# Performance work log

Hardware: AMD Instinct MI355X
Metric: run time of the kernel (lower is better)

The kernel has to match this reference:

```python
import jax, jax.numpy as jnp
import numpy as np

B, S, H, D = 16, 64, 16, 16          # batch, seq, heads, head_dim
E = H * D                             # 256
HID = 128                             # attn_hidden_dim


def setup_inputs() -> dict:
    key = jax.random.key(0)
    ks = jax.random.split(key, 12)
    g = lambda k, sh, s: (jax.random.normal(k, sh, dtype=jnp.float32) * s)
    sE = 1.0 / np.sqrt(E)
    s2d = 1.0 / np.sqrt(2 * D)
    sSD = 1.0 / np.sqrt(S * D)
    return {
        "x": jax.random.normal(ks[0], (B, S, E), dtype=jnp.float32),
        "Wq": g(ks[1], (E, E), sE), "bq": g(ks[2], (E,), sE),
        "Wk": g(ks[3], (E, E), sE), "bk": g(ks[4], (E,), sE),
        "Wv": g(ks[5], (E, E), sE), "bv": g(ks[6], (E,), sE),
        "Wa": g(ks[7], (HID, 2 * D), s2d), "ba": g(ks[8], (HID,), s2d),
        "attn_v": jax.random.normal(ks[9], (HID,), dtype=jnp.float32),
        "Wfc": g(ks[10], (E, S * D), sSD), "bfc": g(ks[11], (E,), sSD),
    }


def reference(x, Wq, bq, Wk, bk, Wv, bv, Wa, ba, attn_v, Wfc, bfc):
    b, s, e = x.shape
    q = (x @ Wq.T + bq).reshape(b, s, H, D)
    k = (x @ Wk.T + bk).reshape(b, s, H, D)
    v = (x @ Wv.T + bv).reshape(b, s, H, D)
    # attn_fc(concat(q_i, k_j)) == q_i @ Wa[:, :D].T + k_j @ Wa[:, D:].T + ba
    pre_q = jnp.einsum('bihd,cd->bihc', q, Wa[:, :D]) + ba   # [B,S,H,HID]
    pre_k = jnp.einsum('bjhd,cd->bjhc', k, Wa[:, D:])        # [B,S,H,HID]
    # scores[b,i,j,h] = tanh(pre_q + pre_k) . attn_v
    t = jnp.tanh(pre_q[:, :, None, :, :] + pre_k[:, None, :, :, :])  # [B,S,S,H,HID]
    scores = jnp.einsum('bijhc,c->bijh', t, attn_v)                   # [B,S,S,H]
    w = jax.nn.softmax(scores, axis=2)                                # softmax over key dim
    # faithful to torch.matmul(w[B,S,S,H], v[B,S,H,D]) -> contracts heads
    ctx = jnp.einsum('bqkh,bqhd->bqkd', w, v).reshape(b, s, s * D)    # [B,S,S*D]
    return ctx @ Wfc.T + bfc                                          # [B,S,E]
```

## Files before the change

### kernel.cpp

```cpp
#include <hip/hip_runtime.h>

#define BB 16
#define SS 64
#define HH 16
#define DD 16
#define EE 256
#define HIDD 128

typedef float f32x4 __attribute__((ext_vector_type(4)));

#define K2CONST 2.8853900817779268f
#define L2E 1.4426950408889634f

#define WQ_OFF 0
#define WK_OFF 4160
#define WV_OFF 8320
#define WA_OFF 12480
#define EQT_OFF 17088
#define EKL_OFF 25408
#define QL_OFF 33856
#define KL_OFF 35136
#define AV2_OFF 36416
#define KBA_OFF 36544
#define SM_TOT 36672
#define SL_OFF 0

__global__ __launch_bounds__(512) void k1(
    const float* __restrict__ x,
    const float* __restrict__ Wq, const float* __restrict__ bq,
    const float* __restrict__ Wk, const float* __restrict__ bk,
    const float* __restrict__ Wv, const float* __restrict__ bv,
    const float* __restrict__ Wa, const float* __restrict__ ba,
    const float* __restrict__ attnv,
    float* __restrict__ v_ws, float* __restrict__ w_ws)
{
  __shared__ float sm[SM_TOT];
  const int t = threadIdx.x;
  const int bid = blockIdx.x;
  const int b = bid >> 4;
  const int h = bid & (HH - 1);

  for (int idx = t; idx < 16 * EE; idx += 512) {
    const int r = idx >> 8;
    const int e = idx & 255;
    const size_t g = (size_t)(h * DD + r) * EE + e;
    sm[WQ_OFF + r * 260 + e] = Wq[g];
    sm[WK_OFF + r * 260 + e] = Wk[g];
    sm[WV_OFF + r * 260 + e] = Wv[g];
  }
  for (int idx = t; idx < HIDD * 2 * DD; idx += 512)
    sm[WA_OFF + (idx >> 5) * 36 + (idx & 31)] = Wa[idx];
  if (t < HIDD) {
    sm[AV2_OFF + t] = 2.0f * attnv[t];
    sm[KBA_OFF + t] = K2CONST * ba[t];
  }
  __syncthreads();

  {
    const int i = t >> 3;
    const int dl = t & 7;
    float aq0 = 0.f, aq1 = 0.f, ak0 = 0.f, ak1 = 0.f, av0 = 0.f, av1 = 0.f;
    const float* xr = x + (size_t)(b * SS + i) * EE;
    const float* wq0 = &sm[WQ_OFF + dl * 260];
    const float* wq1 = &sm[WQ_OFF + (dl + 8) * 260];
    const float* wk0 = &sm[WK_OFF + dl * 260];
    const float* wk1 = &sm[WK_OFF + (dl + 8) * 260];
    const float* wv0 = &sm[WV_OFF + dl * 260];
    const float* wv1 = &sm[WV_OFF + (dl + 8) * 260];
#pragma unroll 4
    for (int e = 0; e < EE; e += 4) {
      const f32x4 x4 = *(const f32x4*)(xr + e);
      const f32x4 q04 = *(const f32x4*)(wq0 + e);
      const f32x4 q14 = *(const f32x4*)(wq1 + e);
      const f32x4 k04 = *(const f32x4*)(wk0 + e);
      const f32x4 k14 = *(const f32x4*)(wk1 + e);
      const f32x4 v04 = *(const f32x4*)(wv0 + e);
      const f32x4 v14 = *(const f32x4*)(wv1 + e);
#pragma unroll
      for (int u = 0; u < 4; ++u) {
        aq0 = fmaf(x4[u], q04[u], aq0);
        aq1 = fmaf(x4[u], q14[u], aq1);
        ak0 = fmaf(x4[u], k04[u], ak0);
        ak1 = fmaf(x4[u], k14[u], ak1);
        av0 = fmaf(x4[u], v04[u], av0);
        av1 = fmaf(x4[u], v14[u], av1);
      }
    }
    sm[QL_OFF + i * 20 + dl]     = aq0 + bq[h * DD + dl];
    sm[QL_OFF + i * 20 + dl + 8] = aq1 + bq[h * DD + dl + 8];
    sm[KL_OFF + i * 20 + dl]     = ak0 + bk[h * DD + dl];
    sm[KL_OFF + i * 20 + dl + 8] = ak1 + bk[h * DD + dl + 8];
    v_ws[(size_t)(b * SS + i) * EE + h * DD + dl]     = av0 + bv[h * DD + dl];
    v_ws[(size_t)(b * SS + i) * EE + h * DD + dl + 8] = av1 + bv[h * DD + dl + 8];
  }
  __syncthreads();

  {
    const int i = t >> 3;
    const int cg = t & 7;
    f32x4 q4[4], k4[4];
#pragma unroll
    for (int u = 0; u < 4; ++u) {
      q4[u] = *(const f32x4*)&sm[QL_OFF + i * 20 + u * 4];
      k4[u] = *(const f32x4*)&sm[KL_OFF + i * 20 + u * 4];
    }
#pragma unroll 2
    for (int jj = 0; jj < 16; ++jj) {
      const int c = cg + 8 * jj;
      const float* war = &sm[WA_OFF + c * 36];
      float sq = 0.f, sk = 0.f;
#pragma unroll
      for (int u = 0; u < 4; ++u) {
        const f32x4 a4 = *(const f32x4*)(war + u * 4);
        const f32x4 b4 = *(const f32x4*)(war + 16 + u * 4);
#pragma unroll
        for (int w = 0; w < 4; ++w) {
          sq = fmaf(q4[u][w], a4[w], sq);
          sk = fmaf(k4[u][w], b4[w], sk);
        }
      }
      const float eq = __builtin_amdgcn_exp2f(fmaf(K2CONST, sq, sm[KBA_OFF + c]));
      const float ek = __builtin_amdgcn_exp2f(K2CONST * sk);
      sm[EQT_OFF + c * 65 + i] = eq;
      sm[EKL_OFF + i * 132 + c] = ek;
    }
  }
  __syncthreads();

  {
    const int i = t & 63;
    const int j0 = (t >> 6) << 3;
    float acc[8];
#pragma unroll
    for (int jj = 0; jj < 8; ++jj) acc[jj] = 0.f;
#pragma unroll 2
    for (int c = 0; c < HIDD; c += 4) {
      const f32x4 a4 = *(const f32x4*)&sm[AV2_OFF + c];
      float eq[4];
#pragma unroll
      for (int u = 0; u < 4; ++u) eq[u] = sm[EQT_OFF + (c + u) * 65 + i];
      f32x4 ek[8];
#pragma unroll
      for (int jj = 0; jj < 8; ++jj) ek[jj] = *(const f32x4*)&sm[EKL_OFF + (j0 + jj) * 132 + c];
#pragma unroll
      for (int u = 0; u < 4; ++u) {
#pragma unroll
        for (int jj = 0; jj < 8; ++jj) {
          const float r = __builtin_amdgcn_rcpf(fmaf(eq[u], ek[jj][u], 1.f));
          acc[jj] = fmaf(a4[u], r, acc[jj]);
        }
      }
    }
#pragma unroll
    for (int jj = 0; jj < 8; ++jj) sm[SL_OFF + i * 65 + j0 + jj] = -acc[jj];
  }
  __syncthreads();

  {
    const int row = t >> 3;
    const int l8 = t & 7;
    float v[8];
#pragma unroll
    for (int jj = 0; jj < 8; ++jj) v[jj] = sm[SL_OFF + row * 65 + l8 * 8 + jj];
    float m = v[0];
#pragma unroll
    for (int jj = 1; jj < 8; ++jj) m = fmaxf(m, v[jj]);
    m = fmaxf(m, __shfl_xor(m, 1));
    m = fmaxf(m, __shfl_xor(m, 2));
    m = fmaxf(m, __shfl_xor(m, 4));
    float p[8], sum = 0.f;
#pragma unroll
    for (int jj = 0; jj < 8; ++jj) {
      p[jj] = __builtin_amdgcn_exp2f((v[jj] - m) * L2E);
      sum += p[jj];
    }
    sum += __shfl_xor(sum, 1);
    sum += __shfl_xor(sum, 2);
    sum += __shfl_xor(sum, 4);
    const float rs = __builtin_amdgcn_rcpf(sum);
    float* wr = w_ws + ((size_t)bid * SS + row) * SS + l8 * 8;
    f32x4 o0, o1;
#pragma unroll
    for (int u = 0; u < 4; ++u) { o0[u] = p[u] * rs; o1[u] = p[4 + u] * rs; }
    *(f32x4*)(wr) = o0;
    *(f32x4*)(wr + 4) = o1;
  }
}

__global__ __launch_bounds__(512) void k2(
    const float* __restrict__ w_ws, const float* __restrict__ v_ws,
    const float* __restrict__ Wfc, const float* __restrict__ bfc,
    float* __restrict__ out)
{
  __shared__ float wl[4 * HH * SS];
  __shared__ float vl[4 * 272];
  __shared__ float ctx[4 * 1024];
  const int t = threadIdx.x;
  const int row0 = blockIdx.x * 4;
  const int b = row0 >> 6;
  const int i0 = row0 & 63;

#pragma unroll
  for (int u = 0; u < 8; ++u) {
    const int idx = t + 512 * u;
    const int r = idx >> 10;
    const int rem = idx & 1023;
    const int h = rem >> 6;
    const int j = rem & 63;
    wl[idx] = w_ws[(((size_t)b * HH + h) * SS + i0 + r) * SS + j];
  }
#pragma unroll
  for (int u = 0; u < 2; ++u) {
    const int idx = t + 512 * u;
    const int r = idx >> 8;
    const int rem = idx & 255;
    vl[r * 272 + (rem >> 4) * 17 + (rem & 15)] = v_ws[(size_t)(row0 + r) * EE + rem];
  }
  __syncthreads();

#pragma unroll
  for (int u = 0; u < 8; ++u) {
    const int o = t + 512 * u;
    const int r = o >> 10;
    const int rem = o & 1023;
    const int j = rem >> 4;
    const int d = rem & 15;
    float s = 0.f;
#pragma unroll
    for (int h = 0; h < HH; ++h)
      s = fmaf(wl[r * 1024 + h * SS + j], vl[r * 272 + h * 17 + d], s);
    ctx[o] = s;
  }
  __syncthreads();

  {
    const int wave = t >> 6;
    const int lane = t & 63;
    const int kg = lane & 15;
    const int eg = lane >> 4;
#pragma unroll 2
    for (int outer = 0; outer < 8; ++outer) {
      const int e = wave * 32 + outer * 4 + eg;
      const float* wfr = Wfc + (size_t)e * (SS * DD);
      float a0 = 0.f, a1 = 0.f, a2 = 0.f, a3 = 0.f;
#pragma unroll 4
      for (int p = 0; p < 16; ++p) {
        const int k0 = p * 64 + kg * 4;
        const f32x4 wf = *(const f32x4*)(wfr + k0);
        const f32x4 c0 = *(const f32x4*)(ctx + k0);
        const f32x4 c1 = *(const f32x4*)(ctx + 1024 + k0);
        const f32x4 c2 = *(const f32x4*)(ctx + 2048 + k0);
        const f32x4 c3 = *(const f32x4*)(ctx + 3072 + k0);
#pragma unroll
        for (int u = 0; u < 4; ++u) {
          a0 = fmaf(wf[u], c0[u], a0);
          a1 = fmaf(wf[u], c1[u], a1);
          a2 = fmaf(wf[u], c2[u], a2);
          a3 = fmaf(wf[u], c3[u], a3);
        }
      }
#pragma unroll
      for (int msk = 1; msk <= 8; msk <<= 1) {
        a0 += __shfl_xor(a0, msk);
        a1 += __shfl_xor(a1, msk);
        a2 += __shfl_xor(a2, msk);
        a3 += __shfl_xor(a3, msk);
      }
      if (kg == 0) {
        const float bias = bfc[e];
        out[(size_t)(row0 + 0) * EE + e] = a0 + bias;
        out[(size_t)(row0 + 1) * EE + e] = a1 + bias;
        out[(size_t)(row0 + 2) * EE + e] = a2 + bias;
        out[(size_t)(row0 + 3) * EE + e] = a3 + bias;
      }
    }
  }
}

extern "C" void kernel_launch(void* const* d_in, const int* in_sizes, int n_in,
                              void* d_out, int out_size, void* d_ws, size_t ws_size,
                              hipStream_t stream) {
  const float* x   = (const float*)d_in[0];
  const float* Wq  = (const float*)d_in[1];
  const float* bq  = (const float*)d_in[2];
  const float* Wk  = (const float*)d_in[3];
  const float* bk  = (const float*)d_in[4];
  const float* Wv  = (const float*)d_in[5];
  const float* bv  = (const float*)d_in[6];
  const float* Wa  = (const float*)d_in[7];
  const float* ba  = (const float*)d_in[8];
  const float* av  = (const float*)d_in[9];
  const float* Wfc = (const float*)d_in[10];
  const float* bfc = (const float*)d_in[11];

  float* ws = (float*)d_ws;
  float* v_ws = ws;
  float* w_ws = v_ws + (size_t)BB * SS * EE;

  hipLaunchKernelGGL(k1, dim3(BB * HH), dim3(512), 0, stream,
                     x, Wq, bq, Wk, bk, Wv, bv, Wa, ba, av, v_ws, w_ws);
  hipLaunchKernelGGL(k2, dim3(BB * SS / 4), dim3(512), 0, stream,
                     w_ws, v_ws, Wfc, bfc, (float*)d_out);
}
```

Before: 129.4 us.

## Shrink k1 LDS, fuse softmax in-register, transpose w store, batch Wfc loads in k2

k1 no longer stages Wa in shared memory; it reads Wa directly from global memory. It overlaps the attention-score buffers with the weight region and sets launch_bounds to 4 blocks per CU to raise occupancy. The softmax now runs on the score accumulators using cross-wave max and sum through small shared arrays, which removes one store/reload pass. w is written transposed so k2 can read it with vector loads. k2's output GEMM keeps 32 accumulators per thread and reloads ctx once per k-step, which increases register pressure in exchange for fewer LDS reads.

```diff
diff --git a/kernel.cpp b/kernel.cpp
--- a/kernel.cpp
+++ b/kernel.cpp
@@ -15,17 +15,17 @@
 #define WQ_OFF 0
 #define WK_OFF 4160
 #define WV_OFF 8320
-#define WA_OFF 12480
-#define EQT_OFF 17088
-#define EKL_OFF 25408
-#define QL_OFF 33856
-#define KL_OFF 35136
-#define AV2_OFF 36416
-#define KBA_OFF 36544
-#define SM_TOT 36672
-#define SL_OFF 0
-
-__global__ __launch_bounds__(512) void k1(
+#define EQT_OFF 0
+#define EKL_OFF 8320
+#define QL_OFF 16768
+#define KL_OFF 18048
+#define PMX_OFF 16768
+#define PSUM_OFF 17344
+#define AV2_OFF 19328
+#define KBA_OFF 19456
+#define SM_TOT 19584
+
+__global__ __launch_bounds__(512, 4) void k1(
     const float* __restrict__ x,
     const float* __restrict__ Wq, const float* __restrict__ bq,
     const float* __restrict__ Wk, const float* __restrict__ bk,
@@ -48,8 +48,6 @@
     sm[WK_OFF + r * 260 + e] = Wk[g];
     sm[WV_OFF + r * 260 + e] = Wv[g];
   }
-  for (int idx = t; idx < HIDD * 2 * DD; idx += 512)
-    sm[WA_OFF + (idx >> 5) * 36 + (idx & 31)] = Wa[idx];
   if (t < HIDD) {
     sm[AV2_OFF + t] = 2.0f * attnv[t];
     sm[KBA_OFF + t] = K2CONST * ba[t];
@@ -107,12 +105,12 @@
 #pragma unroll 2
     for (int jj = 0; jj < 16; ++jj) {
       const int c = cg + 8 * jj;
-      const float* war = &sm[WA_OFF + c * 36];
+      const f32x4* war = (const f32x4*)(Wa + (size_t)c * 32);
       float sq = 0.f, sk = 0.f;
 #pragma unroll
       for (int u = 0; u < 4; ++u) {
-        const f32x4 a4 = *(const f32x4*)(war + u * 4);
-        const f32x4 b4 = *(const f32x4*)(war + 16 + u * 4);
+        const f32x4 a4 = war[u];
+        const f32x4 b4 = war[4 + u];
 #pragma unroll
         for (int w = 0; w < 4; ++w) {
           sq = fmaf(q4[u][w], a4[w], sq);
@@ -129,7 +127,8 @@
 
   {
     const int i = t & 63;
-    const int j0 = (t >> 6) << 3;
+    const int wv = t >> 6;
+    const int j0 = wv << 3;
     float acc[8];
 #pragma unroll
     for (int jj = 0; jj < 8; ++jj) acc[jj] = 0.f;
@@ -151,39 +150,29 @@
         }
       }
     }
-#pragma unroll
-    for (int jj = 0; jj < 8; ++jj) sm[SL_OFF + i * 65 + j0 + jj] = -acc[jj];
-  }
-  __syncthreads();
-
-  {
-    const int row = t >> 3;
-    const int l8 = t & 7;
-    float v[8];
-#pragma unroll
-    for (int jj = 0; jj < 8; ++jj) v[jj] = sm[SL_OFF + row * 65 + l8 * 8 + jj];
-    float m = v[0];
-#pragma unroll
-    for (int jj = 1; jj < 8; ++jj) m = fmaxf(m, v[jj]);
-    m = fmaxf(m, __shfl_xor(m, 1));
-    m = fmaxf(m, __shfl_xor(m, 2));
-    m = fmaxf(m, __shfl_xor(m, 4));
-    float p[8], sum = 0.f;
+    float lm = -acc[0];
+#pragma unroll
+    for (int jj = 1; jj < 8; ++jj) lm = fmaxf(lm, -acc[jj]);
+    sm[PMX_OFF + i * 9 + wv] = lm;
+    __syncthreads();
+    float gm = sm[PMX_OFF + i * 9];
+#pragma unroll
+    for (int w = 1; w < 8; ++w) gm = fmaxf(gm, sm[PMX_OFF + i * 9 + w]);
+    float p[8], ls = 0.f;
 #pragma unroll
     for (int jj = 0; jj < 8; ++jj) {
-      p[jj] = __builtin_amdgcn_exp2f((v[jj] - m) * L2E);
-      sum += p[jj];
-    }
-    sum += __shfl_xor(sum, 1);
-    sum += __shfl_xor(sum, 2);
-    sum += __shfl_xor(sum, 4);
-    const float rs = __builtin_amdgcn_rcpf(sum);
-    float* wr = w_ws + ((size_t)bid * SS + row) * SS + l8 * 8;
-    f32x4 o0, o1;
-#pragma unroll
-    for (int u = 0; u < 4; ++u) { o0[u] = p[u] * rs; o1[u] = p[4 + u] * rs; }
-    *(f32x4*)(wr) = o0;
-    *(f32x4*)(wr + 4) = o1;
+      p[jj] = __builtin_amdgcn_exp2f((-acc[jj] - gm) * L2E);
+      ls += p[jj];
+    }
+    sm[PSUM_OFF + i * 9 + wv] = ls;
+    __syncthreads();
+    float tot = sm[PSUM_OFF + i * 9];
+#pragma unroll
+    for (int w = 1; w < 8; ++w) tot += sm[PSUM_OFF + i * 9 + w];
+    const float rs = __builtin_amdgcn_rcpf(tot);
+#pragma unroll
+    for (int jj = 0; jj < 8; ++jj)
+      w_ws[((size_t)bid * SS + j0 + jj) * SS + i] = p[jj] * rs;
   }
 }
 
@@ -192,7 +181,7 @@
     const float* __restrict__ Wfc, const float* __restrict__ bfc,
     float* __restrict__ out)
 {
-  __shared__ float wl[4 * HH * SS];
+  __shared__ float wl[4 * 1024];
   __shared__ float vl[4 * 272];
   __shared__ float ctx[4 * 1024];
   const int t = threadIdx.x;
@@ -201,13 +190,15 @@
   const int i0 = row0 & 63;
 
 #pragma unroll
-  for (int u = 0; u < 8; ++u) {
+  for (int u = 0; u < 2; ++u) {
     const int idx = t + 512 * u;
-    const int r = idx >> 10;
-    const int rem = idx & 1023;
-    const int h = rem >> 6;
-    const int j = rem & 63;
-    wl[idx] = w_ws[(((size_t)b * HH + h) * SS + i0 + r) * SS + j];
+    const int hh = idx >> 6;
+    const int j = idx & 63;
+    const f32x4 v4 = *(const f32x4*)&w_ws[(((size_t)b * HH + hh) * SS + j) * SS + i0];
+    wl[0 * 1024 + hh * 64 + j] = v4[0];
+    wl[1 * 1024 + hh * 64 + j] = v4[1];
+    wl[2 * 1024 + hh * 64 + j] = v4[2];
+    wl[3 * 1024 + hh * 64 + j] = v4[3];
   }
 #pragma unroll
   for (int u = 0; u < 2; ++u) {
@@ -227,51 +218,58 @@
     const int d = rem & 15;
     float s = 0.f;
 #pragma unroll
-    for (int h = 0; h < HH; ++h)
-      s = fmaf(wl[r * 1024 + h * SS + j], vl[r * 272 + h * 17 + d], s);
+    for (int hh = 0; hh < HH; ++hh)
+      s = fmaf(wl[r * 1024 + hh * 64 + j], vl[r * 272 + hh * 17 + d], s);
     ctx[o] = s;
   }
   __syncthreads();
 
   {
+    const int lane = t & 63;
     const int wave = t >> 6;
-    const int lane = t & 63;
     const int kg = lane & 15;
     const int eg = lane >> 4;
-#pragma unroll 2
-    for (int outer = 0; outer < 8; ++outer) {
-      const int e = wave * 32 + outer * 4 + eg;
-      const float* wfr = Wfc + (size_t)e * (SS * DD);
-      float a0 = 0.f, a1 = 0.f, a2 = 0.f, a3 = 0.f;
-#pragma unroll 4
-      for (int p = 0; p < 16; ++p) {
-        const int k0 = p * 64 + kg * 4;
-        const f32x4 wf = *(const f32x4*)(wfr + k0);
-        const f32x4 c0 = *(const f32x4*)(ctx + k0);
-        const f32x4 c1 = *(const f32x4*)(ctx + 1024 + k0);
-        const f32x4 c2 = *(const f32x4*)(ctx + 2048 + k0);
-        const f32x4 c3 = *(const f32x4*)(ctx + 3072 + k0);
+    float acc[8][4];
+#pragma unroll
+    for (int off = 0; off < 8; ++off)
+#pragma unroll
+      for (int r = 0; r < 4; ++r) acc[off][r] = 0.f;
+
+    for (int p = 0; p < 16; ++p) {
+      const int k0 = p * 64 + kg * 4;
+      const f32x4 c0 = *(const f32x4*)(ctx + k0);
+      const f32x4 c1 = *(const f32x4*)(ctx + 1024 + k0);
+      const f32x4 c2 = *(const f32x4*)(ctx + 2048 + k0);
+      const f32x4 c3 = *(const f32x4*)(ctx + 3072 + k0);
+#pragma unroll
+      for (int off = 0; off < 8; ++off) {
+        const int e = wave * 32 + off * 4 + eg;
+        const f32x4 wf = *(const f32x4*)&Wfc[(size_t)e * (SS * DD) + k0];
 #pragma unroll
         for (int u = 0; u < 4; ++u) {
-          a0 = fmaf(wf[u], c0[u], a0);
-          a1 = fmaf(wf[u], c1[u], a1);
-          a2 = fmaf(wf[u], c2[u], a2);
-          a3 = fmaf(wf[u], c3[u], a3);
+          acc[off][0] = fmaf(wf[u], c0[u], acc[off][0]);
+          acc[off][1] = fmaf(wf[u], c1[u], acc[off][1]);
+          acc[off][2] = fmaf(wf[u], c2[u], acc[off][2]);
+          acc[off][3] = fmaf(wf[u], c3[u], acc[off][3]);
         }
       }
-#pragma unroll
-      for (int msk = 1; msk <= 8; msk <<= 1) {
-        a0 += __shfl_xor(a0, msk);
-        a1 += __shfl_xor(a1, msk);
-        a2 += __shfl_xor(a2, msk);
-        a3 += __shfl_xor(a3, msk);
-      }
-      if (kg == 0) {
+    }
+#pragma unroll
+    for (int off = 0; off < 8; ++off)
+#pragma unroll
+      for (int r = 0; r < 4; ++r) {
+#pragma unroll
+        for (int msk = 1; msk <= 8; msk <<= 1)
+          acc[off][r] += __shfl_xor(acc[off][r], msk);
+      }
+    if (kg == 0) {
+#pragma unroll
+      for (int off = 0; off < 8; ++off) {
+        const int e = wave * 32 + off * 4 + eg;
         const float bias = bfc[e];
-        out[(size_t)(row0 + 0) * EE + e] = a0 + bias;
-        out[(size_t)(row0 + 1) * EE + e] = a1 + bias;
-        out[(size_t)(row0 + 2) * EE + e] = a2 + bias;
-        out[(size_t)(row0 + 3) * EE + e] = a3 + bias;
+#pragma unroll
+        for (int r = 0; r < 4; ++r)
+          out[(size_t)(row0 + r) * EE + e] = acc[off][r] + bias;
       }
     }
   }
```

Measured after the change: 182.1 us. 40.7% more time.
